# Kernel optimization log

Measured on AMD Instinct MI355X. Metric: run time of the kernel, lower is better.

Reference implementation:

```python
import jax, jax.numpy as jnp
import numpy as np

MARGIN = 1.0
EPS = 1e-6  # matches torch F.pairwise_distance eps added to the difference

def setup_inputs() -> dict:
    key = jax.random.key(0)
    k1, k2 = jax.random.split(key)
    B, D = 4096, 768
    embeddings = jax.random.normal(k1, (B, D), dtype=jnp.float32)
    labels = jax.random.randint(k2, (B,), 0, 6, dtype=jnp.int64)
    return {"embeddings": embeddings, "labels": labels,
            "depression_idx": 1, "suicidal_idx": 2}

def reference(embeddings, labels, depression_idx, suicidal_idx):
    # masks over the batch for the two classes
    dep_mask = (labels == depression_idx).astype(embeddings.dtype)  # [B]
    sui_mask = (labels == suicidal_idx).astype(embeddings.dtype)    # [B]

    # torch pairwise_distance computes ||d - s + eps||_2; shift the left side.
    d = embeddings + EPS                                             # [B, D]
    s = embeddings                                                   # [B, D]
    # squared distances via ||d||^2 + ||s||^2 - 2 d.s (single GEMM)
    d2 = jnp.sum(d * d, axis=-1)                                     # [B]
    s2 = jnp.sum(s * s, axis=-1)                                     # [B]
    dist2 = d2[:, None] + s2[None, :] - 2.0 * (d @ s.T)              # [B, B]
    dist = jnp.sqrt(jnp.maximum(dist2, 1e-12))                       # [B, B]

    hinge = jnp.maximum(MARGIN - dist, 0.0)                          # clamp(min=0)
    pair_mask = dep_mask[:, None] * sui_mask[None, :]                # [B, B]
    total = jnp.sum(hinge * pair_mask)
    count = jnp.sum(pair_mask)
    # mean over (depression, suicidal) pairs; 0.0 if either class is empty
    return jnp.where(count > 0, total / jnp.maximum(count, 1.0),
                     jnp.zeros((), embeddings.dtype))
```

## Files before the change

### kernel.cpp

```cpp
#include <hip/hip_runtime.h>
#include <hip/hip_bf16.h>

#define DIM   768
#define KITER (DIM / 32)
#define EPSF  1e-6f
#define MAXB  4096
#define NPB   256

typedef __attribute__((ext_vector_type(4))) float f32x4;
typedef __attribute__((ext_vector_type(8))) short short8;
typedef __attribute__((ext_vector_type(4))) unsigned short ushort4_t;

#define OFF_D2A   64
#define OFF_S2B   (64 + 16384)
#define OFF_PART  (64 + 32768)
#define OFF_IDXA  (64 + 32768 + 4096)
#define OFF_IDXB  (OFF_IDXA + 16384)
#define OFF_BF    (OFF_IDXB + 16384)
#define NEED_COMP ((size_t)OFF_BF + 2ull * MAXB * DIM * 2ull)

__device__ __forceinline__ unsigned short f2bf(float f) {
    return __builtin_bit_cast(unsigned short, __float2bfloat16(f));
}

__device__ __forceinline__ float hinge_from_d2(float dist2) {
    float dist = sqrtf(fmaxf(dist2, 1e-12f));
    return fmaxf(1.0f - dist, 0.0f);
}

template <bool ADD_EPS>
__device__ __forceinline__ short8 load_frag(const float* __restrict__ p) {
    const float4 u = *reinterpret_cast<const float4*>(p);
    const float4 v = *reinterpret_cast<const float4*>(p + 4);
    short8 f;
    if constexpr (ADD_EPS) {
        f[0] = (short)f2bf(u.x + EPSF); f[1] = (short)f2bf(u.y + EPSF);
        f[2] = (short)f2bf(u.z + EPSF); f[3] = (short)f2bf(u.w + EPSF);
        f[4] = (short)f2bf(v.x + EPSF); f[5] = (short)f2bf(v.y + EPSF);
        f[6] = (short)f2bf(v.z + EPSF); f[7] = (short)f2bf(v.w + EPSF);
    } else {
        f[0] = (short)f2bf(u.x); f[1] = (short)f2bf(u.y);
        f[2] = (short)f2bf(u.z); f[3] = (short)f2bf(u.w);
        f[4] = (short)f2bf(v.x); f[5] = (short)f2bf(v.y);
        f[6] = (short)f2bf(v.z); f[7] = (short)f2bf(v.w);
    }
    return f;
}

template <bool COMP>
__global__ void k_norms(const float* __restrict__ emb,
                        const int* __restrict__ labels,
                        const int* __restrict__ depi,
                        const int* __restrict__ suii,
                        int* __restrict__ cnt,
                        int* __restrict__ idxA, int* __restrict__ idxB,
                        float* __restrict__ d2A, float* __restrict__ s2B,
                        unsigned short* __restrict__ Abf,
                        unsigned short* __restrict__ Bbf, int nrows)
{
    const int row  = blockIdx.x * 4 + (threadIdx.x >> 6);
    const int lane = threadIdx.x & 63;
    if (row >= nrows) return;
    const int dep = depi[0], sui = suii[0];
    const int lab = labels[row];
    const bool isA = (lab == dep), isB = (lab == sui);
    const bool isLast = (row == nrows - 1);
    if (!(isA | isB) && !isLast) return;

    int packed = 0;
    for (int j = lane; j < row; j += 64) {
        const int l = labels[j];
        packed += (l == dep) + ((l == sui) << 16);
    }
    #pragma unroll
    for (int off = 32; off; off >>= 1) packed += __shfl_xor(packed, off);
    const int pA = packed & 0xFFFF;
    const int pB = packed >> 16;
    if (isLast && lane == 0) {
        cnt[0] = pA + (isA ? 1 : 0);
        cnt[1] = pB + (isB ? 1 : 0);
    }
    if (!(isA | isB)) return;

    const float* rp = emb + (size_t)row * DIM;
    float4 v[3];
    float s2 = 0.f, d2 = 0.f;
    #pragma unroll
    for (int c = 0; c < 3; ++c) {
        v[c] = *reinterpret_cast<const float4*>(rp + c * 256 + lane * 4);
        s2 += v[c].x * v[c].x + v[c].y * v[c].y + v[c].z * v[c].z + v[c].w * v[c].w;
        const float dx = v[c].x + EPSF, dy = v[c].y + EPSF;
        const float dz = v[c].z + EPSF, dw = v[c].w + EPSF;
        d2 += dx * dx + dy * dy + dz * dz + dw * dw;
    }
    int pk2 = __builtin_bit_cast(int, s2);
    float d2r = d2;
    #pragma unroll
    for (int off = 32; off; off >>= 1) {
        pk2 = __builtin_bit_cast(int,
              __builtin_bit_cast(float, pk2) + __shfl_xor(__builtin_bit_cast(float, pk2), off));
        d2r += __shfl_xor(d2r, off);
    }
    const float s2t = __builtin_bit_cast(float, pk2);

    if (isA) {
        if (lane == 0) { d2A[pA] = d2r; idxA[pA] = row; }
        if constexpr (COMP) {
            unsigned short* dst = Abf + (size_t)pA * DIM;
            #pragma unroll
            for (int c = 0; c < 3; ++c) {
                ushort4_t wd;
                wd[0] = f2bf(v[c].x + EPSF); wd[1] = f2bf(v[c].y + EPSF);
                wd[2] = f2bf(v[c].z + EPSF); wd[3] = f2bf(v[c].w + EPSF);
                *reinterpret_cast<ushort4_t*>(dst + c * 256 + lane * 4) = wd;
            }
        }
    }
    if (isB) {
        if (lane == 0) { s2B[pB] = s2t; idxB[pB] = row; }
        if constexpr (COMP) {
            unsigned short* dst = Bbf + (size_t)pB * DIM;
            #pragma unroll
            for (int c = 0; c < 3; ++c) {
                ushort4_t wd;
                wd[0] = f2bf(v[c].x); wd[1] = f2bf(v[c].y);
                wd[2] = f2bf(v[c].z); wd[3] = f2bf(v[c].w);
                *reinterpret_cast<ushort4_t*>(dst + c * 256 + lane * 4) = wd;
            }
        }
    }
}

template <bool COMP>
__global__ void __launch_bounds__(256)
k_pairs(const float* __restrict__ emb,
        const int* __restrict__ cnt,
        const float* __restrict__ d2A, const float* __restrict__ s2B,
        const int* __restrict__ idxA, const int* __restrict__ idxB,
        const unsigned short* __restrict__ Abf,
        const unsigned short* __restrict__ Bbf,
        float* __restrict__ partials)
{
    __shared__ float wsum[4];
    const int nA = cnt[0], nB = cnt[1];
    const unsigned nTi = (unsigned)(nA + 31) >> 5;
    const unsigned nTj = (unsigned)(nB + 31) >> 5;
    const unsigned T   = nTi * nTj;
    const int tid = threadIdx.x, wv = tid >> 6, lane = tid & 63;
    const int r = lane & 15, kq = lane >> 4;
    float wacc = 0.f;

    for (unsigned t = blockIdx.x + wv * gridDim.x; t < T; t += gridDim.x * 4) {
        const unsigned ti = t / nTj;
        const unsigned tj = t - ti * nTj;
        const int a0 = (int)(ti << 5), b0 = (int)(tj << 5);
        const int ar0 = min(a0 + r,      nA - 1);
        const int ar1 = min(a0 + 16 + r, nA - 1);
        const int br0 = min(b0 + r,      nB - 1);
        const int br1 = min(b0 + 16 + r, nB - 1);
        f32x4 acc00 = {0.f,0.f,0.f,0.f}, acc01 = {0.f,0.f,0.f,0.f};
        f32x4 acc10 = {0.f,0.f,0.f,0.f}, acc11 = {0.f,0.f,0.f,0.f};

        if constexpr (COMP) {
            const short8* pa0 = reinterpret_cast<const short8*>(Abf + (size_t)ar0 * DIM) + kq;
            const short8* pa1 = reinterpret_cast<const short8*>(Abf + (size_t)ar1 * DIM) + kq;
            const short8* pb0 = reinterpret_cast<const short8*>(Bbf + (size_t)br0 * DIM) + kq;
            const short8* pb1 = reinterpret_cast<const short8*>(Bbf + (size_t)br1 * DIM) + kq;
            #pragma unroll 6
            for (int kk = 0; kk < KITER; ++kk) {
                const short8 fa0 = pa0[4 * kk], fa1 = pa1[4 * kk];
                const short8 fb0 = pb0[4 * kk], fb1 = pb1[4 * kk];
                acc00 = __builtin_amdgcn_mfma_f32_16x16x32_bf16(fa0, fb0, acc00, 0, 0, 0);
                acc01 = __builtin_amdgcn_mfma_f32_16x16x32_bf16(fa0, fb1, acc01, 0, 0, 0);
                acc10 = __builtin_amdgcn_mfma_f32_16x16x32_bf16(fa1, fb0, acc10, 0, 0, 0);
                acc11 = __builtin_amdgcn_mfma_f32_16x16x32_bf16(fa1, fb1, acc11, 0, 0, 0);
            }
        } else {
            const float* qa0 = emb + (size_t)idxA[ar0] * DIM + kq * 8;
            const float* qa1 = emb + (size_t)idxA[ar1] * DIM + kq * 8;
            const float* qb0 = emb + (size_t)idxB[br0] * DIM + kq * 8;
            const float* qb1 = emb + (size_t)idxB[br1] * DIM + kq * 8;
            #pragma unroll 3
            for (int kk = 0; kk < KITER; ++kk) {
                const short8 fa0 = load_frag<true >(qa0 + 32 * kk);
                const short8 fa1 = load_frag<true >(qa1 + 32 * kk);
                const short8 fb0 = load_frag<false>(qb0 + 32 * kk);
                const short8 fb1 = load_frag<false>(qb1 + 32 * kk);
                acc00 = __builtin_amdgcn_mfma_f32_16x16x32_bf16(fa0, fb0, acc00, 0, 0, 0);
                acc01 = __builtin_amdgcn_mfma_f32_16x16x32_bf16(fa0, fb1, acc01, 0, 0, 0);
                acc10 = __builtin_amdgcn_mfma_f32_16x16x32_bf16(fa1, fb0, acc10, 0, 0, 0);
                acc11 = __builtin_amdgcn_mfma_f32_16x16x32_bf16(fa1, fb1, acc11, 0, 0, 0);
            }
        }

        const int bc0 = b0 + r, bc1 = b0 + 16 + r;
        const float s20 = (bc0 < nB) ? s2B[bc0] : 0.f;
        const float s21 = (bc1 < nB) ? s2B[bc1] : 0.f;
        #pragma unroll
        for (int j = 0; j < 4; ++j) {
            const int arl = a0 + (kq << 2) + j;
            const int arh = arl + 16;
            const float d2l = (arl < nA) ? d2A[arl] : 0.f;
            const float d2h = (arh < nA) ? d2A[arh] : 0.f;
            if (arl < nA && bc0 < nB) wacc += hinge_from_d2(d2l + s20 - 2.f * acc00[j]);
            if (arl < nA && bc1 < nB) wacc += hinge_from_d2(d2l + s21 - 2.f * acc01[j]);
            if (arh < nA && bc0 < nB) wacc += hinge_from_d2(d2h + s20 - 2.f * acc10[j]);
            if (arh < nA && bc1 < nB) wacc += hinge_from_d2(d2h + s21 - 2.f * acc11[j]);
        }
    }

    #pragma unroll
    for (int off = 32; off; off >>= 1) wacc += __shfl_down(wacc, off);
    if (lane == 0) wsum[wv] = wacc;
    __syncthreads();
    if (tid == 0)
        partials[blockIdx.x] = wsum[0] + wsum[1] + wsum[2] + wsum[3];
}

__global__ void __launch_bounds__(NPB)
k_final(const float* __restrict__ partials, const int* __restrict__ cnt,
        float* __restrict__ out)
{
    __shared__ float sm[NPB];
    const int tid = threadIdx.x;
    sm[tid] = partials[tid];
    __syncthreads();
    for (int off = NPB / 2; off; off >>= 1) {
        if (tid < off) sm[tid] += sm[tid + off];
        __syncthreads();
    }
    if (tid == 0) {
        const long long c = (long long)cnt[0] * (long long)cnt[1];
        out[0] = (c > 0) ? sm[0] / (float)c : 0.f;
    }
}

extern "C" void kernel_launch(void* const* d_in, const int* in_sizes, int n_in,
                              void* d_out, int out_size, void* d_ws, size_t ws_size,
                              hipStream_t stream)
{
    const float* emb  = (const float*)d_in[0];
    const int* labels = (const int*)d_in[1];
    const int* depi   = (const int*)d_in[2];
    const int* suii   = (const int*)d_in[3];
    float* out        = (float*)d_out;

    char* ws = (char*)d_ws;
    int*   cnt      = (int*)ws;
    float* d2A      = (float*)(ws + OFF_D2A);
    float* s2B      = (float*)(ws + OFF_S2B);
    float* partials = (float*)(ws + OFF_PART);
    int*   idxA     = (int*)(ws + OFF_IDXA);
    int*   idxB     = (int*)(ws + OFF_IDXB);
    unsigned short* Abf = (unsigned short*)(ws + OFF_BF);
    unsigned short* Bbf = Abf + (size_t)MAXB * DIM;

    const int nrows = in_sizes[0] / DIM;
    const int nblk  = (nrows + 3) / 4;

    if (ws_size >= NEED_COMP) {
        k_norms<true><<<nblk, 256, 0, stream>>>(emb, labels, depi, suii, cnt,
                                                idxA, idxB, d2A, s2B, Abf, Bbf, nrows);
        k_pairs<true><<<NPB, 256, 0, stream>>>(emb, cnt, d2A, s2B, idxA, idxB,
                                               Abf, Bbf, partials);
    } else {
        k_norms<false><<<nblk, 256, 0, stream>>>(emb, labels, depi, suii, cnt,
                                                 idxA, idxB, d2A, s2B, Abf, Bbf, nrows);
        k_pairs<false><<<NPB, 256, 0, stream>>>(emb, cnt, d2A, s2B, idxA, idxB,
                                                Abf, Bbf, partials);
    }
    k_final<<<1, NPB, 0, stream>>>(partials, cnt, out);
}
```

Measured before the change: 26.87 us.

## Fuse norms, pair GEMM and final reduction into one persistent kernel

Merges the three launches into a single persistent kernel of 256 blocks. A global atomic barrier separates the row-compaction/norm phase from the pairwise MFMA phase, and a last-block-done counter performs the final reduction. Each wave now handles a contiguous run of rows, so it does one label prefix scan instead of one scan per row. This removes two kernel launch gaps. In exchange it adds a memset, relies on all 256 blocks being co-resident for the spin barrier, and serialises row processing within each wave.

```diff
diff --git a/kernel.cpp b/kernel.cpp
--- a/kernel.cpp
+++ b/kernel.cpp
@@ -5,16 +5,18 @@
 #define KITER (DIM / 32)
 #define EPSF  1e-6f
 #define MAXB  4096
-#define NPB   256
+#define NBLK  256
+#define NTHR  256
 
 typedef __attribute__((ext_vector_type(4))) float f32x4;
 typedef __attribute__((ext_vector_type(8))) short short8;
 typedef __attribute__((ext_vector_type(4))) unsigned short ushort4_t;
 
-#define OFF_D2A   64
-#define OFF_S2B   (64 + 16384)
-#define OFF_PART  (64 + 32768)
-#define OFF_IDXA  (64 + 32768 + 4096)
+#define OFF_CNT   64
+#define OFF_PART  128
+#define OFF_D2A   1152
+#define OFF_S2B   (OFF_D2A + 16384)
+#define OFF_IDXA  (OFF_S2B + 16384)
 #define OFF_IDXB  (OFF_IDXA + 16384)
 #define OFF_BF    (OFF_IDXB + 16384)
 #define NEED_COMP ((size_t)OFF_BF + 2ull * MAXB * DIM * 2ull)
@@ -48,109 +50,108 @@
 }
 
 template <bool COMP>
-__global__ void k_norms(const float* __restrict__ emb,
-                        const int* __restrict__ labels,
-                        const int* __restrict__ depi,
-                        const int* __restrict__ suii,
-                        int* __restrict__ cnt,
-                        int* __restrict__ idxA, int* __restrict__ idxB,
-                        float* __restrict__ d2A, float* __restrict__ s2B,
-                        unsigned short* __restrict__ Abf,
-                        unsigned short* __restrict__ Bbf, int nrows)
-{
-    const int row  = blockIdx.x * 4 + (threadIdx.x >> 6);
-    const int lane = threadIdx.x & 63;
-    if (row >= nrows) return;
-    const int dep = depi[0], sui = suii[0];
-    const int lab = labels[row];
-    const bool isA = (lab == dep), isB = (lab == sui);
-    const bool isLast = (row == nrows - 1);
-    if (!(isA | isB) && !isLast) return;
-
-    int packed = 0;
-    for (int j = lane; j < row; j += 64) {
-        const int l = labels[j];
-        packed += (l == dep) + ((l == sui) << 16);
-    }
-    #pragma unroll
-    for (int off = 32; off; off >>= 1) packed += __shfl_xor(packed, off);
-    const int pA = packed & 0xFFFF;
-    const int pB = packed >> 16;
-    if (isLast && lane == 0) {
-        cnt[0] = pA + (isA ? 1 : 0);
-        cnt[1] = pB + (isB ? 1 : 0);
-    }
-    if (!(isA | isB)) return;
-
-    const float* rp = emb + (size_t)row * DIM;
-    float4 v[3];
-    float s2 = 0.f, d2 = 0.f;
-    #pragma unroll
-    for (int c = 0; c < 3; ++c) {
-        v[c] = *reinterpret_cast<const float4*>(rp + c * 256 + lane * 4);
-        s2 += v[c].x * v[c].x + v[c].y * v[c].y + v[c].z * v[c].z + v[c].w * v[c].w;
-        const float dx = v[c].x + EPSF, dy = v[c].y + EPSF;
-        const float dz = v[c].z + EPSF, dw = v[c].w + EPSF;
-        d2 += dx * dx + dy * dy + dz * dz + dw * dw;
-    }
-    int pk2 = __builtin_bit_cast(int, s2);
-    float d2r = d2;
-    #pragma unroll
-    for (int off = 32; off; off >>= 1) {
-        pk2 = __builtin_bit_cast(int,
-              __builtin_bit_cast(float, pk2) + __shfl_xor(__builtin_bit_cast(float, pk2), off));
-        d2r += __shfl_xor(d2r, off);
-    }
-    const float s2t = __builtin_bit_cast(float, pk2);
-
-    if (isA) {
-        if (lane == 0) { d2A[pA] = d2r; idxA[pA] = row; }
-        if constexpr (COMP) {
-            unsigned short* dst = Abf + (size_t)pA * DIM;
-            #pragma unroll
-            for (int c = 0; c < 3; ++c) {
-                ushort4_t wd;
-                wd[0] = f2bf(v[c].x + EPSF); wd[1] = f2bf(v[c].y + EPSF);
-                wd[2] = f2bf(v[c].z + EPSF); wd[3] = f2bf(v[c].w + EPSF);
-                *reinterpret_cast<ushort4_t*>(dst + c * 256 + lane * 4) = wd;
-            }
-        }
-    }
-    if (isB) {
-        if (lane == 0) { s2B[pB] = s2t; idxB[pB] = row; }
-        if constexpr (COMP) {
-            unsigned short* dst = Bbf + (size_t)pB * DIM;
-            #pragma unroll
-            for (int c = 0; c < 3; ++c) {
-                ushort4_t wd;
-                wd[0] = f2bf(v[c].x); wd[1] = f2bf(v[c].y);
-                wd[2] = f2bf(v[c].z); wd[3] = f2bf(v[c].w);
-                *reinterpret_cast<ushort4_t*>(dst + c * 256 + lane * 4) = wd;
-            }
-        }
-    }
-}
-
-template <bool COMP>
-__global__ void __launch_bounds__(256)
-k_pairs(const float* __restrict__ emb,
-        const int* __restrict__ cnt,
-        const float* __restrict__ d2A, const float* __restrict__ s2B,
-        const int* __restrict__ idxA, const int* __restrict__ idxB,
-        const unsigned short* __restrict__ Abf,
-        const unsigned short* __restrict__ Bbf,
-        float* __restrict__ partials)
+__global__ void __launch_bounds__(NTHR)
+k_fused(const float* __restrict__ emb,
+        const int* __restrict__ labels,
+        const int* __restrict__ depi, const int* __restrict__ suii,
+        unsigned* __restrict__ bar1, unsigned* __restrict__ bar2,
+        int* __restrict__ cnt,
+        float* __restrict__ d2A, float* __restrict__ s2B,
+        int* __restrict__ idxA, int* __restrict__ idxB,
+        unsigned short* __restrict__ Abf, unsigned short* __restrict__ Bbf,
+        float* __restrict__ partials, float* __restrict__ out, int nrows)
 {
     __shared__ float wsum[4];
+    __shared__ float sm[NTHR];
+    __shared__ int   islast;
+    const int tid = threadIdx.x, lane = tid & 63, wv = tid >> 6;
+    const int gw  = blockIdx.x * 4 + wv;
+    const int dep = depi[0], sui = suii[0];
+
+    const int NW  = NBLK * 4;
+    const int rpw = (nrows + NW - 1) / NW;
+    const int r0  = gw * rpw;
+    const int r1  = min(r0 + rpw, nrows);
+    if (r0 < nrows) {
+        int packed = 0;
+        for (int j = lane; j < r0; j += 64) {
+            const int l = labels[j];
+            packed += (l == dep) + ((l == sui) << 16);
+        }
+        #pragma unroll
+        for (int off = 32; off; off >>= 1) packed += __shfl_xor(packed, off);
+        int pA = packed & 0xFFFF, pB = packed >> 16;
+
+        for (int row = r0; row < r1; ++row) {
+            const int lab = labels[row];
+            const bool isA = (lab == dep), isB = (lab == sui);
+            if (isA | isB) {
+                const float* rp = emb + (size_t)row * DIM;
+                float4 v[3];
+                float s2 = 0.f, d2 = 0.f;
+                #pragma unroll
+                for (int c = 0; c < 3; ++c) {
+                    v[c] = *reinterpret_cast<const float4*>(rp + c * 256 + lane * 4);
+                    s2 += v[c].x * v[c].x + v[c].y * v[c].y
+                        + v[c].z * v[c].z + v[c].w * v[c].w;
+                    const float dx = v[c].x + EPSF, dy = v[c].y + EPSF;
+                    const float dz = v[c].z + EPSF, dw = v[c].w + EPSF;
+                    d2 += dx * dx + dy * dy + dz * dz + dw * dw;
+                }
+                #pragma unroll
+                for (int off = 32; off; off >>= 1) {
+                    s2 += __shfl_xor(s2, off);
+                    d2 += __shfl_xor(d2, off);
+                }
+                if (isA) {
+                    if (lane == 0) { d2A[pA] = d2; idxA[pA] = row; }
+                    if constexpr (COMP) {
+                        unsigned short* dst = Abf + (size_t)pA * DIM;
+                        #pragma unroll
+                        for (int c = 0; c < 3; ++c) {
+                            ushort4_t wd;
+                            wd[0] = f2bf(v[c].x + EPSF); wd[1] = f2bf(v[c].y + EPSF);
+                            wd[2] = f2bf(v[c].z + EPSF); wd[3] = f2bf(v[c].w + EPSF);
+                            *reinterpret_cast<ushort4_t*>(dst + c * 256 + lane * 4) = wd;
+                        }
+                    }
+                }
+                if (isB) {
+                    if (lane == 0) { s2B[pB] = s2; idxB[pB] = row; }
+                    if constexpr (COMP) {
+                        unsigned short* dst = Bbf + (size_t)pB * DIM;
+                        #pragma unroll
+                        for (int c = 0; c < 3; ++c) {
+                            ushort4_t wd;
+                            wd[0] = f2bf(v[c].x); wd[1] = f2bf(v[c].y);
+                            wd[2] = f2bf(v[c].z); wd[3] = f2bf(v[c].w);
+                            *reinterpret_cast<ushort4_t*>(dst + c * 256 + lane * 4) = wd;
+                        }
+                    }
+                }
+                pA += isA; pB += isB;
+            }
+            if (row == nrows - 1 && lane == 0) { cnt[0] = pA; cnt[1] = pB; }
+        }
+    }
+
+    __syncthreads();
+    if (tid == 0) {
+        __hip_atomic_fetch_add(bar1, 1u, __ATOMIC_ACQ_REL, __HIP_MEMORY_SCOPE_AGENT);
+        while (__hip_atomic_load(bar1, __ATOMIC_ACQUIRE, __HIP_MEMORY_SCOPE_AGENT)
+               < (unsigned)gridDim.x)
+            __builtin_amdgcn_s_sleep(1);
+    }
+    __syncthreads();
+
     const int nA = cnt[0], nB = cnt[1];
     const unsigned nTi = (unsigned)(nA + 31) >> 5;
     const unsigned nTj = (unsigned)(nB + 31) >> 5;
     const unsigned T   = nTi * nTj;
-    const int tid = threadIdx.x, wv = tid >> 6, lane = tid & 63;
-    const int r = lane & 15, kq = lane >> 4;
+    const int r  = lane & 15, kq = lane >> 4;
     float wacc = 0.f;
 
-    for (unsigned t = blockIdx.x + wv * gridDim.x; t < T; t += gridDim.x * 4) {
+    for (unsigned t = (unsigned)gw; t < T; t += (unsigned)(NBLK * 4)) {
         const unsigned ti = t / nTj;
         const unsigned tj = t - ti * nTj;
         const int a0 = (int)(ti << 5), b0 = (int)(tj << 5);
@@ -213,25 +214,25 @@
     for (int off = 32; off; off >>= 1) wacc += __shfl_down(wacc, off);
     if (lane == 0) wsum[wv] = wacc;
     __syncthreads();
-    if (tid == 0)
+    if (tid == 0) {
         partials[blockIdx.x] = wsum[0] + wsum[1] + wsum[2] + wsum[3];
-}
-
-__global__ void __launch_bounds__(NPB)
-k_final(const float* __restrict__ partials, const int* __restrict__ cnt,
-        float* __restrict__ out)
-{
-    __shared__ float sm[NPB];
-    const int tid = threadIdx.x;
-    sm[tid] = partials[tid];
-    __syncthreads();
-    for (int off = NPB / 2; off; off >>= 1) {
-        if (tid < off) sm[tid] += sm[tid + off];
+        const unsigned old = __hip_atomic_fetch_add(bar2, 1u, __ATOMIC_ACQ_REL,
+                                                    __HIP_MEMORY_SCOPE_AGENT);
+        islast = (old == (unsigned)gridDim.x - 1) ? 1 : 0;
+    }
+    __syncthreads();
+
+    if (islast) {
+        sm[tid] = (tid < NBLK) ? partials[tid] : 0.f;
         __syncthreads();
-    }
-    if (tid == 0) {
-        const long long c = (long long)cnt[0] * (long long)cnt[1];
-        out[0] = (c > 0) ? sm[0] / (float)c : 0.f;
+        for (int off = NTHR / 2; off; off >>= 1) {
+            if (tid < off) sm[tid] += sm[tid + off];
+            __syncthreads();
+        }
+        if (tid == 0) {
+            const long long c = (long long)nA * (long long)nB;
+            out[0] = (c > 0) ? sm[0] / (float)c : 0.f;
+        }
     }
 }
 
@@ -246,28 +247,27 @@
     float* out        = (float*)d_out;
 
     char* ws = (char*)d_ws;
-    int*   cnt      = (int*)ws;
+    unsigned* bar1  = (unsigned*)ws;
+    unsigned* bar2  = (unsigned*)(ws + 4);
+    int*   cnt      = (int*)(ws + OFF_CNT);
+    float* partials = (float*)(ws + OFF_PART);
     float* d2A      = (float*)(ws + OFF_D2A);
     float* s2B      = (float*)(ws + OFF_S2B);
-    float* partials = (float*)(ws + OFF_PART);
     int*   idxA     = (int*)(ws + OFF_IDXA);
     int*   idxB     = (int*)(ws + OFF_IDXB);
     unsigned short* Abf = (unsigned short*)(ws + OFF_BF);
     unsigned short* Bbf = Abf + (size_t)MAXB * DIM;
 
     const int nrows = in_sizes[0] / DIM;
-    const int nblk  = (nrows + 3) / 4;
-
+
+    hipMemsetAsync(ws, 0, 16, stream);
     if (ws_size >= NEED_COMP) {
-        k_norms<true><<<nblk, 256, 0, stream>>>(emb, labels, depi, suii, cnt,
-                                                idxA, idxB, d2A, s2B, Abf, Bbf, nrows);
-        k_pairs<true><<<NPB, 256, 0, stream>>>(emb, cnt, d2A, s2B, idxA, idxB,
-                                               Abf, Bbf, partials);
+        k_fused<true><<<NBLK, NTHR, 0, stream>>>(
+            emb, labels, depi, suii, bar1, bar2, cnt, d2A, s2B, idxA, idxB,
+            Abf, Bbf, partials, out, nrows);
     } else {
-        k_norms<false><<<nblk, 256, 0, stream>>>(emb, labels, depi, suii, cnt,
-                                                 idxA, idxB, d2A, s2B, Abf, Bbf, nrows);
-        k_pairs<false><<<NPB, 256, 0, stream>>>(emb, cnt, d2A, s2B, idxA, idxB,
-                                                Abf, Bbf, partials);
-    }
-    k_final<<<1, NPB, 0, stream>>>(partials, cnt, out);
-}
+        k_fused<false><<<NBLK, NTHR, 0, stream>>>(
+            emb, labels, depi, suii, bar1, bar2, cnt, d2A, s2B, idxA, idxB,
+            Abf, Bbf, partials, out, nrows);
+    }
+}
```

New measurement: 70.06 us. 2.61x slower.

## Fuse final reduction into pair kernel via last-block atomic counter

Applied to the files above, without the earlier changes.

Removes the separate single-block final reduction kernel. Each pair block now publishes its partial with a release store and bumps a global counter, and the last block to arrive reduces all partials and writes the mean. The pair-kernel grid also doubles to 512 blocks for more parallelism, and a memset that resets the counter is added to the stream. This trades one kernel launch for an extra memset plus atomic traffic.

```diff
diff --git a/kernel.cpp b/kernel.cpp
--- a/kernel.cpp
+++ b/kernel.cpp
@@ -5,7 +5,7 @@
 #define KITER (DIM / 32)
 #define EPSF  1e-6f
 #define MAXB  4096
-#define NPB   256
+#define NPB   512
 
 typedef __attribute__((ext_vector_type(4))) float f32x4;
 typedef __attribute__((ext_vector_type(8))) short short8;
@@ -14,7 +14,7 @@
 #define OFF_D2A   64
 #define OFF_S2B   (64 + 16384)
 #define OFF_PART  (64 + 32768)
-#define OFF_IDXA  (64 + 32768 + 4096)
+#define OFF_IDXA  (OFF_PART + 4096)
 #define OFF_IDXB  (OFF_IDXA + 16384)
 #define OFF_BF    (OFF_IDXB + 16384)
 #define NEED_COMP ((size_t)OFF_BF + 2ull * MAXB * DIM * 2ull)
@@ -93,15 +93,12 @@
         const float dz = v[c].z + EPSF, dw = v[c].w + EPSF;
         d2 += dx * dx + dy * dy + dz * dz + dw * dw;
     }
-    int pk2 = __builtin_bit_cast(int, s2);
-    float d2r = d2;
+    float s2r = s2, d2r = d2;
     #pragma unroll
     for (int off = 32; off; off >>= 1) {
-        pk2 = __builtin_bit_cast(int,
-              __builtin_bit_cast(float, pk2) + __shfl_xor(__builtin_bit_cast(float, pk2), off));
+        s2r += __shfl_xor(s2r, off);
         d2r += __shfl_xor(d2r, off);
     }
-    const float s2t = __builtin_bit_cast(float, pk2);
 
     if (isA) {
         if (lane == 0) { d2A[pA] = d2r; idxA[pA] = row; }
@@ -117,7 +114,7 @@
         }
     }
     if (isB) {
-        if (lane == 0) { s2B[pB] = s2t; idxB[pB] = row; }
+        if (lane == 0) { s2B[pB] = s2r; idxB[pB] = row; }
         if constexpr (COMP) {
             unsigned short* dst = Bbf + (size_t)pB * DIM;
             #pragma unroll
@@ -139,9 +136,13 @@
         const int* __restrict__ idxA, const int* __restrict__ idxB,
         const unsigned short* __restrict__ Abf,
         const unsigned short* __restrict__ Bbf,
-        float* __restrict__ partials)
+        float* __restrict__ partials,
+        unsigned* __restrict__ done,
+        float* __restrict__ out)
 {
     __shared__ float wsum[4];
+    __shared__ float sm[256];
+    __shared__ int   islast;
     const int nA = cnt[0], nB = cnt[1];
     const unsigned nTi = (unsigned)(nA + 31) >> 5;
     const unsigned nTj = (unsigned)(nB + 31) >> 5;
@@ -213,25 +214,31 @@
     for (int off = 32; off; off >>= 1) wacc += __shfl_down(wacc, off);
     if (lane == 0) wsum[wv] = wacc;
     __syncthreads();
-    if (tid == 0)
-        partials[blockIdx.x] = wsum[0] + wsum[1] + wsum[2] + wsum[3];
-}
-
-__global__ void __launch_bounds__(NPB)
-k_final(const float* __restrict__ partials, const int* __restrict__ cnt,
-        float* __restrict__ out)
-{
-    __shared__ float sm[NPB];
-    const int tid = threadIdx.x;
-    sm[tid] = partials[tid];
+    if (tid == 0) {
+        __hip_atomic_store(&partials[blockIdx.x],
+                           wsum[0] + wsum[1] + wsum[2] + wsum[3],
+                           __ATOMIC_RELEASE, __HIP_MEMORY_SCOPE_AGENT);
+        const unsigned old = __hip_atomic_fetch_add(done, 1u, __ATOMIC_ACQ_REL,
+                                                    __HIP_MEMORY_SCOPE_AGENT);
+        islast = (old == (unsigned)gridDim.x - 1) ? 1 : 0;
+    }
     __syncthreads();
-    for (int off = NPB / 2; off; off >>= 1) {
-        if (tid < off) sm[tid] += sm[tid + off];
+
+    if (islast) {
+        float s = 0.f;
+        for (int i = tid; i < (int)gridDim.x; i += 256)
+            s += __hip_atomic_load(&partials[i], __ATOMIC_RELAXED,
+                                   __HIP_MEMORY_SCOPE_AGENT);
+        sm[tid] = s;
         __syncthreads();
-    }
-    if (tid == 0) {
-        const long long c = (long long)cnt[0] * (long long)cnt[1];
-        out[0] = (c > 0) ? sm[0] / (float)c : 0.f;
+        for (int off = 128; off; off >>= 1) {
+            if (tid < off) sm[tid] += sm[tid + off];
+            __syncthreads();
+        }
+        if (tid == 0) {
+            const long long c = (long long)nA * (long long)nB;
+            out[0] = (c > 0) ? sm[0] / (float)c : 0.f;
+        }
     }
 }
 
@@ -246,28 +253,29 @@
     float* out        = (float*)d_out;
 
     char* ws = (char*)d_ws;
-    int*   cnt      = (int*)ws;
-    float* d2A      = (float*)(ws + OFF_D2A);
-    float* s2B      = (float*)(ws + OFF_S2B);
-    float* partials = (float*)(ws + OFF_PART);
-    int*   idxA     = (int*)(ws + OFF_IDXA);
-    int*   idxB     = (int*)(ws + OFF_IDXB);
+    int*      cnt      = (int*)ws;
+    unsigned* done     = (unsigned*)(ws + 8);
+    float*    d2A      = (float*)(ws + OFF_D2A);
+    float*    s2B      = (float*)(ws + OFF_S2B);
+    float*    partials = (float*)(ws + OFF_PART);
+    int*      idxA     = (int*)(ws + OFF_IDXA);
+    int*      idxB     = (int*)(ws + OFF_IDXB);
     unsigned short* Abf = (unsigned short*)(ws + OFF_BF);
     unsigned short* Bbf = Abf + (size_t)MAXB * DIM;
 
     const int nrows = in_sizes[0] / DIM;
     const int nblk  = (nrows + 3) / 4;
 
+    hipMemsetAsync(ws + 8, 0, 4, stream);
     if (ws_size >= NEED_COMP) {
         k_norms<true><<<nblk, 256, 0, stream>>>(emb, labels, depi, suii, cnt,
                                                 idxA, idxB, d2A, s2B, Abf, Bbf, nrows);
         k_pairs<true><<<NPB, 256, 0, stream>>>(emb, cnt, d2A, s2B, idxA, idxB,
-                                               Abf, Bbf, partials);
+                                               Abf, Bbf, partials, done, out);
     } else {
         k_norms<false><<<nblk, 256, 0, stream>>>(emb, labels, depi, suii, cnt,
                                                  idxA, idxB, d2A, s2B, Abf, Bbf, nrows);
         k_pairs<false><<<NPB, 256, 0, stream>>>(emb, cnt, d2A, s2B, idxA, idxB,
-                                                Abf, Bbf, partials);
-    }
-    k_final<<<1, NPB, 0, stream>>>(partials, cnt, out);
-}
+                                                Abf, Bbf, partials, done, out);
+    }
+}
```

New measurement: 43.16 us. 1.61x slower.
